# Kernel tuning notes

Hardware: AMD Instinct MI355X
Metric: run time of the kernel (lower is better)

## Reference

```python
import jax, jax.numpy as jnp
import numpy as np

KSIZE = 9
SIGMA = 7.0
ALPHA = 0.05
POOL = 7


def _conv(x, w, pad):
    # x: (N, Cin, H, W), w: (Cout, Cin, kh, kw), zero padding, stride 1
    return jax.lax.conv_general_dilated(
        x, w, window_strides=(1, 1), padding=[(pad, pad), (pad, pad)],
        dimension_numbers=("NCHW", "OIHW", "NCHW"))


def setup_inputs() -> dict:
    key = jax.random.key(0)
    x = jax.random.normal(key, (4, 1, 2048, 2048), dtype=jnp.float32)
    # Sobel filters (ImageGradientsLayer): out ch 0 = Ix, out ch 1 = Iy
    sobel_w = jnp.array(
        [[[[-1., 0., 1.], [-2., 0., 2.], [-1., 0., 1.]]],
         [[[-1., -2., -1.], [0., 0., 0.], [1., 2., 1.]]]], dtype=jnp.float32)
    # Normalized 2D Gaussian kernel, ksize=9, sigma=7
    ax = np.arange(KSIZE) - (KSIZE - 1) / 2.0
    g1 = np.exp(-(ax ** 2) / (2.0 * SIGMA ** 2))
    g2 = np.outer(g1, g1)
    g2 = g2 / g2.sum()
    gauss_w = jnp.asarray(g2, dtype=jnp.float32)[None, None]  # (1,1,9,9)
    return {"x": x, "sobel_w": sobel_w, "gauss_w": gauss_w}


def reference(x, sobel_w, gauss_w):
    # 1) ImageGradientsLayer: Sobel conv -> (N, 2, H, W)
    g = _conv(x, sobel_w, 1)
    Ix, Iy = g[:, 0], g[:, 1]
    # 2) ChannelProductLayer: I_xx, I_yy, I_xy -> (N, 3, H, W)
    prods = jnp.stack([Ix * Ix, Iy * Iy, Ix * Iy], axis=1)
    # 3) SecondMomentMatrixLayer: same 9x9 Gaussian on each channel
    N, C, H, W = prods.shape
    S = _conv(prods.reshape(N * C, 1, H, W), gauss_w, (KSIZE - 1) // 2)
    S = S.reshape(N, C, H, W)
    # 4) CornerResponseLayer: R = det - alpha * trace^2
    det = S[:, 0] * S[:, 1] - S[:, 2] * S[:, 2]
    tr = S[:, 0] + S[:, 1]
    R = (det - ALPHA * tr * tr)[:, None]  # (N, 1, H, W)
    # 5) NMSLayer: global (lower) median threshold, 7x7 maxpool, equality mask
    n = R.size
    med = jnp.sort(R.reshape(-1))[(n - 1) // 2]  # torch.median = lower median
    xt = jnp.where(R > med, R, jnp.zeros_like(R))
    pad = (POOL - 1) // 2
    y = jax.lax.reduce_window(
        xt, -jnp.inf, jax.lax.max, (1, 1, POOL, POOL), (1, 1, 1, 1),
        [(0, 0), (0, 0), (pad, pad), (pad, pad)])
    mask = (xt == y).astype(xt.dtype)
    return mask * xt
```

## Files before the change

### kernel.cpp

```cpp
#include <hip/hip_runtime.h>
#include <cstdint>
#include <math.h>

#define IMH 2048
#define IMW 2048
#define NB 4
#define NPIX (NB*IMH*IMW)
#define MEDRANK ((NPIX-1)/2)
#define ALPHA 0.05f

#define TW 64
#define TH 24
#define XROWS (TH+10)
#define XSTR 84
#define HROWS (TH+8)
#define HSTR 68

__device__ __forceinline__ uint32_t fkey(float f){
  uint32_t u = __float_as_uint(f);
  return (u & 0x80000000u) ? ~u : (u | 0x80000000u);
}
__device__ __forceinline__ uint32_t aload(const uint32_t* p){
  return __hip_atomic_load(p, __ATOMIC_RELAXED, __HIP_MEMORY_SCOPE_AGENT);
}
__device__ __forceinline__ float ldz(const float* __restrict__ p, int r, int c){
  return (r >= 0 && r < IMH && c >= 0 && c < IMW) ? p[(size_t)r*IMW + c] : 0.f;
}

__global__ __launch_bounds__(256) void harris_front(
    const float* __restrict__ x, const float* __restrict__ gauss_w,
    float* __restrict__ R)
{
  __shared__ float xs[XROWS][XSTR];
  __shared__ float hs[3][HROWS][HSTR];

  const int tid = threadIdx.x;
  const int C0 = blockIdx.x * TW;
  const int R0 = blockIdx.y * TH;
  const int n  = blockIdx.z;
  const float* xb = x + (size_t)n * (size_t)(IMH*IMW);

  float ga[9];
  {
    float a4 = sqrtf(gauss_w[4*9+4]);
#pragma unroll
    for (int i = 0; i < 9; i++) ga[i] = gauss_w[4*9+i] / a4;
  }

  for (int u = tid; u < XROWS*20; u += 256){
    int r = u / 20, c4 = u % 20;
    int gr = R0 - 5 + r;
    int gc = C0 - 8 + c4*4;
    float4 v;
    if (gr >= 0 && gr < IMH && gc >= 0 && gc + 3 < IMW){
      v = *reinterpret_cast<const float4*>(&xb[(size_t)gr*IMW + gc]);
    } else {
      v.x = ldz(xb, gr, gc+0); v.y = ldz(xb, gr, gc+1);
      v.z = ldz(xb, gr, gc+2); v.w = ldz(xb, gr, gc+3);
    }
    *reinterpret_cast<float4*>(&xs[r][c4*4]) = v;
  }
  __syncthreads();

  {
    const int hr = tid >> 3;
    const int oc = (tid & 7) * 8;
    const int gr = R0 - 4 + hr;
    const bool rowv = ((unsigned)gr < (unsigned)IMH);

    float ix[16], iy[16];
    {
      float sv[24], dv[24];
#pragma unroll
      for (int m = 0; m < 6; m++){
        float4 a = *reinterpret_cast<const float4*>(&xs[hr  ][oc + m*4]);
        float4 b = *reinterpret_cast<const float4*>(&xs[hr+1][oc + m*4]);
        float4 c = *reinterpret_cast<const float4*>(&xs[hr+2][oc + m*4]);
        sv[m*4+0] = fmaf(2.f, b.x, a.x + c.x);  dv[m*4+0] = c.x - a.x;
        sv[m*4+1] = fmaf(2.f, b.y, a.y + c.y);  dv[m*4+1] = c.y - a.y;
        sv[m*4+2] = fmaf(2.f, b.z, a.z + c.z);  dv[m*4+2] = c.z - a.z;
        sv[m*4+3] = fmaf(2.f, b.w, a.w + c.w);  dv[m*4+3] = c.w - a.w;
      }
#pragma unroll
      for (int j = 0; j < 16; j++){
        float vx = sv[j+5] - sv[j+3];
        float vy = dv[j+3] + fmaf(2.f, dv[j+4], dv[j+5]);
        int gc = C0 + oc - 4 + j;
        bool vld = rowv && ((unsigned)gc < (unsigned)IMW);
        ix[j] = vld ? vx : 0.f;
        iy[j] = vld ? vy : 0.f;
      }
    }
#pragma unroll
    for (int p = 0; p < 3; p++){
      float pr[16];
#pragma unroll
      for (int j = 0; j < 16; j++)
        pr[j] = (p == 0) ? ix[j]*ix[j] : (p == 1) ? iy[j]*iy[j] : ix[j]*iy[j];
      float o[8];
#pragma unroll
      for (int t2 = 0; t2 < 8; t2++){
        float s = 0.f;
#pragma unroll
        for (int k = 0; k < 9; k++) s = fmaf(ga[k], pr[t2+k], s);
        o[t2] = s;
      }
      *reinterpret_cast<float4*>(&hs[p][hr][oc])   = make_float4(o[0],o[1],o[2],o[3]);
      *reinterpret_cast<float4*>(&hs[p][hr][oc+4]) = make_float4(o[4],o[5],o[6],o[7]);
    }
  }
  __syncthreads();

  if (tid < 192){
    const int c4o = tid & 15;
    const int r0o = (tid >> 4) * 2;
    float4 sA[3], sB[3];
#pragma unroll
    for (int p = 0; p < 3; p++){
      float4 a0 = make_float4(0,0,0,0), a1 = make_float4(0,0,0,0);
#pragma unroll
      for (int k = 0; k < 10; k++){
        float4 hv = *reinterpret_cast<const float4*>(&hs[p][r0o+k][c4o*4]);
        if (k < 9){
          a0.x = fmaf(ga[k], hv.x, a0.x); a0.y = fmaf(ga[k], hv.y, a0.y);
          a0.z = fmaf(ga[k], hv.z, a0.z); a0.w = fmaf(ga[k], hv.w, a0.w);
        }
        if (k >= 1){
          a1.x = fmaf(ga[k-1], hv.x, a1.x); a1.y = fmaf(ga[k-1], hv.y, a1.y);
          a1.z = fmaf(ga[k-1], hv.z, a1.z); a1.w = fmaf(ga[k-1], hv.w, a1.w);
        }
      }
      sA[p] = a0; sB[p] = a1;
    }
    float* Rb = R + (size_t)n * (size_t)(IMH*IMW);
    float4 o0, o1;
    float s0, s1, s2, det, tr;
    s0=sA[0].x; s1=sA[1].x; s2=sA[2].x; det=s0*s1-s2*s2; tr=s0+s1; o0.x=det-ALPHA*tr*tr;
    s0=sA[0].y; s1=sA[1].y; s2=sA[2].y; det=s0*s1-s2*s2; tr=s0+s1; o0.y=det-ALPHA*tr*tr;
    s0=sA[0].z; s1=sA[1].z; s2=sA[2].z; det=s0*s1-s2*s2; tr=s0+s1; o0.z=det-ALPHA*tr*tr;
    s0=sA[0].w; s1=sA[1].w; s2=sA[2].w; det=s0*s1-s2*s2; tr=s0+s1; o0.w=det-ALPHA*tr*tr;
    s0=sB[0].x; s1=sB[1].x; s2=sB[2].x; det=s0*s1-s2*s2; tr=s0+s1; o1.x=det-ALPHA*tr*tr;
    s0=sB[0].y; s1=sB[1].y; s2=sB[2].y; det=s0*s1-s2*s2; tr=s0+s1; o1.y=det-ALPHA*tr*tr;
    s0=sB[0].z; s1=sB[1].z; s2=sB[2].z; det=s0*s1-s2*s2; tr=s0+s1; o1.z=det-ALPHA*tr*tr;
    s0=sB[0].w; s1=sB[1].w; s2=sB[2].w; det=s0*s1-s2*s2; tr=s0+s1; o1.w=det-ALPHA*tr*tr;

    const int orow = R0 + r0o;
    const int ocol = C0 + c4o*4;
    if (orow < IMH)
      *reinterpret_cast<float4*>(&Rb[(size_t)orow*IMW + ocol]) = o0;
    if (orow + 1 < IMH)
      *reinterpret_cast<float4*>(&Rb[(size_t)(orow+1)*IMW + ocol]) = o1;
  }
}

#define HREP 32
__global__ __launch_bounds__(256) void harris_hist8(
    const float4* __restrict__ R4, uint32_t* __restrict__ h8,
    uint32_t* __restrict__ state, uint32_t* __restrict__ ctr)
{
  __shared__ uint32_t lh[256*HREP];
  __shared__ uint32_t sc[256];
  __shared__ int lastFlag;
  for (int i = threadIdx.x; i < 256*HREP; i += 256) lh[i] = 0;
  __syncthreads();
  const int copy = threadIdx.x & (HREP-1);
  const int stride = gridDim.x * 256;
  for (int i = blockIdx.x*256 + threadIdx.x; i < NPIX/4; i += stride){
    float4 v = R4[i];
    atomicAdd(&lh[(fkey(v.x) >> 24)*HREP + copy], 1u);
    atomicAdd(&lh[(fkey(v.y) >> 24)*HREP + copy], 1u);
    atomicAdd(&lh[(fkey(v.z) >> 24)*HREP + copy], 1u);
    atomicAdd(&lh[(fkey(v.w) >> 24)*HREP + copy], 1u);
  }
  __syncthreads();
  {
    const int t = threadIdx.x;
    uint32_t s = 0;
#pragma unroll
    for (int i = 0; i < HREP; i++) s += lh[t*HREP + ((t + i) & (HREP-1))];
    if (s) atomicAdd(&h8[t], s);
  }
  __syncthreads();
  if (threadIdx.x == 0){
    __threadfence();
    lastFlag = (atomicAdd(ctr, 1u) == (uint32_t)gridDim.x - 1u);
  }
  __syncthreads();
  if (!lastFlag) return;
  __threadfence();
  const int t = threadIdx.x;
  uint32_t cnt = aload(&h8[t]);
  sc[t] = cnt;
  __syncthreads();
  for (int off = 1; off < 256; off <<= 1){
    uint32_t v = (t >= off) ? sc[t-off] : 0u;
    __syncthreads();
    sc[t] += v;
    __syncthreads();
  }
  uint32_t excl = sc[t] - cnt;
  if ((uint32_t)MEDRANK >= excl && (uint32_t)MEDRANK < excl + cnt){
    state[0] = (uint32_t)t;
    state[1] = (uint32_t)MEDRANK - excl;
  }
}

__global__ __launch_bounds__(256) void harris_hist12(
    const float4* __restrict__ R4, uint32_t* __restrict__ h,
    uint32_t* __restrict__ state, uint32_t* __restrict__ ctr, int phase)
{
  __shared__ uint32_t lh[4096];
  __shared__ uint32_t sc[256];
  __shared__ int lastFlag;
  for (int i = threadIdx.x; i < 4096; i += 256) lh[i] = 0;
  __syncthreads();
  const uint32_t target = (phase == 0) ? state[0] : ((state[0] << 12) | state[2]);
  const int shift = (phase == 0) ? 24 : 12;
  const int stride = gridDim.x * 256;
  for (int i = blockIdx.x*256 + threadIdx.x; i < NPIX/4; i += stride){
    float4 v = R4[i];
    uint32_t k;
    k = fkey(v.x); if ((k >> shift) == target) atomicAdd(&lh[(k >> (shift-12)) & 0xfffu], 1u);
    k = fkey(v.y); if ((k >> shift) == target) atomicAdd(&lh[(k >> (shift-12)) & 0xfffu], 1u);
    k = fkey(v.z); if ((k >> shift) == target) atomicAdd(&lh[(k >> (shift-12)) & 0xfffu], 1u);
    k = fkey(v.w); if ((k >> shift) == target) atomicAdd(&lh[(k >> (shift-12)) & 0xfffu], 1u);
  }
  __syncthreads();
  for (int i = threadIdx.x; i < 4096; i += 256)
    if (lh[i]) atomicAdd(&h[i], lh[i]);
  __syncthreads();
  if (threadIdx.x == 0){
    __threadfence();
    lastFlag = (atomicAdd(ctr, 1u) == (uint32_t)gridDim.x - 1u);
  }
  __syncthreads();
  if (!lastFlag) return;
  __threadfence();
  const int t = threadIdx.x;
  uint32_t vals[16];
  uint32_t lsum = 0;
#pragma unroll
  for (int i = 0; i < 16; i++){ vals[i] = aload(&h[t*16 + i]); lsum += vals[i]; }
  sc[t] = lsum;
  __syncthreads();
  for (int off = 1; off < 256; off <<= 1){
    uint32_t v = (t >= off) ? sc[t-off] : 0u;
    __syncthreads();
    sc[t] += v;
    __syncthreads();
  }
  uint32_t excl = sc[t] - lsum;
  uint32_t rank = (phase == 0) ? state[1] : state[3];
  if (rank >= excl && rank < excl + lsum){
    uint32_t cum = excl;
    for (int i = 0; i < 16; i++){
      if (rank < cum + vals[i]){
        uint32_t bin = (uint32_t)(t*16 + i);
        if (phase == 0){ state[2] = bin; state[3] = rank - cum; }
        else {
          uint32_t key = (state[0] << 24) | (state[2] << 12) | bin;
          uint32_t u = (key & 0x80000000u) ? (key & 0x7fffffffu) : ~key;
          state[4] = u;
        }
        break;
      }
      cum += vals[i];
    }
  }
}

#define PT 64
__global__ __launch_bounds__(256) void harris_nms(
    const float* __restrict__ R, const uint32_t* __restrict__ state,
    float* __restrict__ out)
{
  __shared__ float xt[PT+6][76];
  __shared__ float hm[PT+6][68];

  const int tid = threadIdx.x;
  const int C0 = blockIdx.x * PT;
  const int R0 = blockIdx.y * PT;
  const int n  = blockIdx.z;
  const float med = __uint_as_float(state[4]);
  const float* Rb = R + (size_t)n * (size_t)(IMH*IMW);

  for (int u = tid; u < 70*18; u += 256){
    int r  = u / 18, c4 = u % 18;
    int gr = R0 - 3 + r;
    int gc = C0 - 4 + c4*4;
    float4 v;
    if (gr >= 0 && gr < IMH && gc >= 0 && gc + 3 < IMW){
      v = *reinterpret_cast<const float4*>(&Rb[(size_t)gr*IMW + gc]);
      v.x = v.x > med ? v.x : 0.f;
      v.y = v.y > med ? v.y : 0.f;
      v.z = v.z > med ? v.z : 0.f;
      v.w = v.w > med ? v.w : 0.f;
    } else {
      float t0, t1, t2, t3;
      t0 = (gr>=0&&gr<IMH&&gc+0>=0&&gc+0<IMW) ? Rb[(size_t)gr*IMW+gc+0] : -INFINITY;
      t1 = (gr>=0&&gr<IMH&&gc+1>=0&&gc+1<IMW) ? Rb[(size_t)gr*IMW+gc+1] : -INFINITY;
      t2 = (gr>=0&&gr<IMH&&gc+2>=0&&gc+2<IMW) ? Rb[(size_t)gr*IMW+gc+2] : -INFINITY;
      t3 = (gr>=0&&gr<IMH&&gc+3>=0&&gc+3<IMW) ? Rb[(size_t)gr*IMW+gc+3] : -INFINITY;
      v.x = (t0 == -INFINITY) ? t0 : (t0 > med ? t0 : 0.f);
      v.y = (t1 == -INFINITY) ? t1 : (t1 > med ? t1 : 0.f);
      v.z = (t2 == -INFINITY) ? t2 : (t2 > med ? t2 : 0.f);
      v.w = (t3 == -INFINITY) ? t3 : (t3 > med ? t3 : 0.f);
    }
    *reinterpret_cast<float4*>(&xt[r][c4*4]) = v;
  }
  __syncthreads();

  for (int u = tid; u < 70*16; u += 256){
    int r = u / 16, c4 = u % 16;
    float4 t0 = *reinterpret_cast<const float4*>(&xt[r][c4*4]);
    float4 t1 = *reinterpret_cast<const float4*>(&xt[r][c4*4+4]);
    float4 t2 = *reinterpret_cast<const float4*>(&xt[r][c4*4+8]);
    float w[12];
    w[0]=t0.x; w[1]=t0.y; w[2]=t0.z; w[3]=t0.w;
    w[4]=t1.x; w[5]=t1.y; w[6]=t1.z; w[7]=t1.w;
    w[8]=t2.x; w[9]=t2.y; w[10]=t2.z; w[11]=t2.w;
    float o[4];
#pragma unroll
    for (int j = 0; j < 4; j++){
      float m = w[j+1];
#pragma unroll
      for (int k = 2; k <= 7; k++) m = fmaxf(m, w[j+k]);
      o[j] = m;
    }
    *reinterpret_cast<float4*>(&hm[r][c4*4]) = make_float4(o[0],o[1],o[2],o[3]);
  }
  __syncthreads();

  const int c4o = tid & 15;
  const int r0o = (tid >> 4) * 4;
  float4 hv[10];
#pragma unroll
  for (int k = 0; k < 10; k++)
    hv[k] = *reinterpret_cast<const float4*>(&hm[r0o+k][c4o*4]);

  float* ob = out + (size_t)n * (size_t)(IMH*IMW);
#pragma unroll
  for (int i = 0; i < 4; i++){
    float4 y = hv[i];
#pragma unroll
    for (int k = 1; k < 7; k++){
      float4 t = hv[i+k];
      y.x = fmaxf(y.x, t.x); y.y = fmaxf(y.y, t.y);
      y.z = fmaxf(y.z, t.z); y.w = fmaxf(y.w, t.w);
    }
    float4 c = *reinterpret_cast<const float4*>(&xt[r0o+i+3][c4o*4+4]);
    float4 o;
    o.x = (c.x == y.x) ? c.x : 0.f;
    o.y = (c.y == y.y) ? c.y : 0.f;
    o.z = (c.z == y.z) ? c.z : 0.f;
    o.w = (c.w == y.w) ? c.w : 0.f;
    *reinterpret_cast<float4*>(&ob[(size_t)(R0+r0o+i)*IMW + C0 + c4o*4]) = o;
  }
}

extern "C" void kernel_launch(void* const* d_in, const int* in_sizes, int n_in,
                              void* d_out, int out_size, void* d_ws, size_t ws_size,
                              hipStream_t stream)
{
  (void)in_sizes; (void)n_in; (void)out_size; (void)ws_size;
  const float* x  = (const float*)d_in[0];
  const float* gw = (const float*)d_in[2];
  float* out = (float*)d_out;

  float* R = (float*)d_ws;
  uint32_t* aux   = (uint32_t*)((char*)d_ws + (size_t)NPIX * sizeof(float));
  uint32_t* h8    = aux;
  uint32_t* h12a  = aux + 256;
  uint32_t* h12b  = aux + 256 + 4096;
  uint32_t* state = aux + 256 + 4096 + 4096;
  uint32_t* ctr   = state + 8;

  hipMemsetAsync(aux, 0, (256 + 4096 + 4096 + 8 + 3) * sizeof(uint32_t), stream);

  harris_front<<<dim3(IMW/TW, (IMH + TH - 1)/TH, NB), 256, 0, stream>>>(x, gw, R);

  harris_hist8 <<<1024, 256, 0, stream>>>((const float4*)R, h8, state, ctr);
  harris_hist12<<<1024, 256, 0, stream>>>((const float4*)R, h12a, state, ctr+1, 0);
  harris_hist12<<<1024, 256, 0, stream>>>((const float4*)R, h12b, state, ctr+2, 1);

  harris_nms<<<dim3(IMW/PT, IMH/PT, NB), 256, 0, stream>>>(R, state, out);
}
```

Measured before the change: 342.8 us.

## Fuse histogram passes and NMS into one persistent kernel with grid barriers

Merges the three radix-select histogram kernels and the NMS kernel into a single persistent kernel of 512 blocks. Blocks synchronise through spin-wait grid barriers on global counters instead of separate launches, and the median search state is carried in registers and shared memory. The histogram loops also process two float4 loads per iteration. This removes the launch gaps between kernels and the last-block-done scan logic, but relies on all 512 blocks being co-resident for the spin barriers, and the 8-tile-per-block NMS loop may reduce parallelism.

```diff
diff --git a/kernel.cpp b/kernel.cpp
--- a/kernel.cpp
+++ b/kernel.cpp
@@ -15,6 +15,9 @@
 #define XSTR 84
 #define HROWS (TH+8)
 #define HSTR 68
+
+#define TB 512
+#define HREP 32
 
 __device__ __forceinline__ uint32_t fkey(float f){
   uint32_t u = __float_as_uint(f);
@@ -153,208 +156,280 @@
   }
 }
 
-#define HREP 32
-__global__ __launch_bounds__(256) void harris_hist8(
-    const float4* __restrict__ R4, uint32_t* __restrict__ h8,
-    uint32_t* __restrict__ state, uint32_t* __restrict__ ctr)
+__global__ __launch_bounds__(256) void harris_tail(
+    const float* __restrict__ R, uint32_t* __restrict__ h8,
+    uint32_t* __restrict__ h12a, uint32_t* __restrict__ h12b,
+    uint32_t* __restrict__ ctr, float* __restrict__ out)
 {
-  __shared__ uint32_t lh[256*HREP];
-  __shared__ uint32_t sc[256];
-  __shared__ int lastFlag;
-  for (int i = threadIdx.x; i < 256*HREP; i += 256) lh[i] = 0;
-  __syncthreads();
-  const int copy = threadIdx.x & (HREP-1);
-  const int stride = gridDim.x * 256;
-  for (int i = blockIdx.x*256 + threadIdx.x; i < NPIX/4; i += stride){
-    float4 v = R4[i];
-    atomicAdd(&lh[(fkey(v.x) >> 24)*HREP + copy], 1u);
-    atomicAdd(&lh[(fkey(v.y) >> 24)*HREP + copy], 1u);
-    atomicAdd(&lh[(fkey(v.z) >> 24)*HREP + copy], 1u);
-    atomicAdd(&lh[(fkey(v.w) >> 24)*HREP + copy], 1u);
-  }
-  __syncthreads();
-  {
-    const int t = threadIdx.x;
+  __shared__ uint32_t sm[10080];
+  uint32_t* lh = sm;
+  uint32_t* sc = sm + 8192;
+  uint32_t* bc = sm + 8448;
+
+  const int tid = threadIdx.x;
+  const int bid = blockIdx.x;
+  const float4* R4 = (const float4*)R;
+  const uint32_t stride = TB * 256;
+
+  for (int i = tid; i < 8192; i += 256) lh[i] = 0;
+  __syncthreads();
+  {
+    const int copy = tid & (HREP-1);
+    for (uint32_t i = bid*256 + tid; i < NPIX/4; i += 2*stride){
+      float4 a = R4[i];
+      float4 b = R4[i + stride];
+      atomicAdd(&lh[(fkey(a.x) >> 24)*HREP + copy], 1u);
+      atomicAdd(&lh[(fkey(a.y) >> 24)*HREP + copy], 1u);
+      atomicAdd(&lh[(fkey(a.z) >> 24)*HREP + copy], 1u);
+      atomicAdd(&lh[(fkey(a.w) >> 24)*HREP + copy], 1u);
+      atomicAdd(&lh[(fkey(b.x) >> 24)*HREP + copy], 1u);
+      atomicAdd(&lh[(fkey(b.y) >> 24)*HREP + copy], 1u);
+      atomicAdd(&lh[(fkey(b.z) >> 24)*HREP + copy], 1u);
+      atomicAdd(&lh[(fkey(b.w) >> 24)*HREP + copy], 1u);
+    }
+  }
+  __syncthreads();
+  {
     uint32_t s = 0;
 #pragma unroll
-    for (int i = 0; i < HREP; i++) s += lh[t*HREP + ((t + i) & (HREP-1))];
-    if (s) atomicAdd(&h8[t], s);
-  }
-  __syncthreads();
-  if (threadIdx.x == 0){
+    for (int i = 0; i < HREP; i++) s += lh[tid*HREP + ((tid + i) & (HREP-1))];
+    if (s) atomicAdd(&h8[tid], s);
+  }
+
+  __syncthreads();
+  if (tid == 0){
     __threadfence();
-    lastFlag = (atomicAdd(ctr, 1u) == (uint32_t)gridDim.x - 1u);
-  }
-  __syncthreads();
-  if (!lastFlag) return;
-  __threadfence();
-  const int t = threadIdx.x;
-  uint32_t cnt = aload(&h8[t]);
-  sc[t] = cnt;
-  __syncthreads();
-  for (int off = 1; off < 256; off <<= 1){
-    uint32_t v = (t >= off) ? sc[t-off] : 0u;
-    __syncthreads();
-    sc[t] += v;
-    __syncthreads();
-  }
-  uint32_t excl = sc[t] - cnt;
-  if ((uint32_t)MEDRANK >= excl && (uint32_t)MEDRANK < excl + cnt){
-    state[0] = (uint32_t)t;
-    state[1] = (uint32_t)MEDRANK - excl;
-  }
-}
-
-__global__ __launch_bounds__(256) void harris_hist12(
-    const float4* __restrict__ R4, uint32_t* __restrict__ h,
-    uint32_t* __restrict__ state, uint32_t* __restrict__ ctr, int phase)
-{
-  __shared__ uint32_t lh[4096];
-  __shared__ uint32_t sc[256];
-  __shared__ int lastFlag;
-  for (int i = threadIdx.x; i < 4096; i += 256) lh[i] = 0;
-  __syncthreads();
-  const uint32_t target = (phase == 0) ? state[0] : ((state[0] << 12) | state[2]);
-  const int shift = (phase == 0) ? 24 : 12;
-  const int stride = gridDim.x * 256;
-  for (int i = blockIdx.x*256 + threadIdx.x; i < NPIX/4; i += stride){
-    float4 v = R4[i];
+    __hip_atomic_fetch_add(ctr, 1u, __ATOMIC_RELEASE, __HIP_MEMORY_SCOPE_AGENT);
+    while (__hip_atomic_load(ctr, __ATOMIC_ACQUIRE, __HIP_MEMORY_SCOPE_AGENT) < (uint32_t)TB)
+      __builtin_amdgcn_s_sleep(2);
+  }
+  __syncthreads();
+
+  uint32_t b1, r1;
+  {
+    uint32_t c = aload(&h8[tid]);
+    sc[tid] = c;
+    __syncthreads();
+    for (int off = 1; off < 256; off <<= 1){
+      uint32_t v = (tid >= off) ? sc[tid-off] : 0u;
+      __syncthreads();
+      sc[tid] += v;
+      __syncthreads();
+    }
+    uint32_t excl = sc[tid] - c;
+    if ((uint32_t)MEDRANK >= excl && (uint32_t)MEDRANK < excl + c){
+      bc[0] = (uint32_t)tid;
+      bc[1] = (uint32_t)MEDRANK - excl;
+    }
+    __syncthreads();
+    b1 = bc[0]; r1 = bc[1];
+  }
+
+  __syncthreads();
+  for (int i = tid; i < 4096; i += 256) lh[i] = 0;
+  __syncthreads();
+  for (uint32_t i = bid*256 + tid; i < NPIX/4; i += 2*stride){
+    float4 a = R4[i];
+    float4 b = R4[i + stride];
     uint32_t k;
-    k = fkey(v.x); if ((k >> shift) == target) atomicAdd(&lh[(k >> (shift-12)) & 0xfffu], 1u);
-    k = fkey(v.y); if ((k >> shift) == target) atomicAdd(&lh[(k >> (shift-12)) & 0xfffu], 1u);
-    k = fkey(v.z); if ((k >> shift) == target) atomicAdd(&lh[(k >> (shift-12)) & 0xfffu], 1u);
-    k = fkey(v.w); if ((k >> shift) == target) atomicAdd(&lh[(k >> (shift-12)) & 0xfffu], 1u);
-  }
-  __syncthreads();
-  for (int i = threadIdx.x; i < 4096; i += 256)
-    if (lh[i]) atomicAdd(&h[i], lh[i]);
-  __syncthreads();
-  if (threadIdx.x == 0){
+    k = fkey(a.x); if ((k >> 24) == b1) atomicAdd(&lh[(k >> 12) & 0xfffu], 1u);
+    k = fkey(a.y); if ((k >> 24) == b1) atomicAdd(&lh[(k >> 12) & 0xfffu], 1u);
+    k = fkey(a.z); if ((k >> 24) == b1) atomicAdd(&lh[(k >> 12) & 0xfffu], 1u);
+    k = fkey(a.w); if ((k >> 24) == b1) atomicAdd(&lh[(k >> 12) & 0xfffu], 1u);
+    k = fkey(b.x); if ((k >> 24) == b1) atomicAdd(&lh[(k >> 12) & 0xfffu], 1u);
+    k = fkey(b.y); if ((k >> 24) == b1) atomicAdd(&lh[(k >> 12) & 0xfffu], 1u);
+    k = fkey(b.z); if ((k >> 24) == b1) atomicAdd(&lh[(k >> 12) & 0xfffu], 1u);
+    k = fkey(b.w); if ((k >> 24) == b1) atomicAdd(&lh[(k >> 12) & 0xfffu], 1u);
+  }
+  __syncthreads();
+  for (int i = tid; i < 4096; i += 256)
+    if (lh[i]) atomicAdd(&h12a[i], lh[i]);
+
+  __syncthreads();
+  if (tid == 0){
     __threadfence();
-    lastFlag = (atomicAdd(ctr, 1u) == (uint32_t)gridDim.x - 1u);
-  }
-  __syncthreads();
-  if (!lastFlag) return;
-  __threadfence();
-  const int t = threadIdx.x;
-  uint32_t vals[16];
-  uint32_t lsum = 0;
-#pragma unroll
-  for (int i = 0; i < 16; i++){ vals[i] = aload(&h[t*16 + i]); lsum += vals[i]; }
-  sc[t] = lsum;
-  __syncthreads();
-  for (int off = 1; off < 256; off <<= 1){
-    uint32_t v = (t >= off) ? sc[t-off] : 0u;
-    __syncthreads();
-    sc[t] += v;
-    __syncthreads();
-  }
-  uint32_t excl = sc[t] - lsum;
-  uint32_t rank = (phase == 0) ? state[1] : state[3];
-  if (rank >= excl && rank < excl + lsum){
-    uint32_t cum = excl;
-    for (int i = 0; i < 16; i++){
-      if (rank < cum + vals[i]){
-        uint32_t bin = (uint32_t)(t*16 + i);
-        if (phase == 0){ state[2] = bin; state[3] = rank - cum; }
-        else {
-          uint32_t key = (state[0] << 24) | (state[2] << 12) | bin;
-          uint32_t u = (key & 0x80000000u) ? (key & 0x7fffffffu) : ~key;
-          state[4] = u;
+    __hip_atomic_fetch_add(ctr+1, 1u, __ATOMIC_RELEASE, __HIP_MEMORY_SCOPE_AGENT);
+    while (__hip_atomic_load(ctr+1, __ATOMIC_ACQUIRE, __HIP_MEMORY_SCOPE_AGENT) < (uint32_t)TB)
+      __builtin_amdgcn_s_sleep(2);
+  }
+  __syncthreads();
+
+  uint32_t b2, r2;
+  {
+    uint32_t vals[16];
+    uint32_t lsum = 0;
+#pragma unroll
+    for (int i = 0; i < 16; i++){ vals[i] = aload(&h12a[tid*16 + i]); lsum += vals[i]; }
+    sc[tid] = lsum;
+    __syncthreads();
+    for (int off = 1; off < 256; off <<= 1){
+      uint32_t v = (tid >= off) ? sc[tid-off] : 0u;
+      __syncthreads();
+      sc[tid] += v;
+      __syncthreads();
+    }
+    uint32_t excl = sc[tid] - lsum;
+    if (r1 >= excl && r1 < excl + lsum){
+      uint32_t cum = excl;
+      for (int i = 0; i < 16; i++){
+        if (r1 < cum + vals[i]){
+          bc[2] = (uint32_t)(tid*16 + i);
+          bc[3] = r1 - cum;
+          break;
         }
-        break;
-      }
-      cum += vals[i];
-    }
-  }
-}
-
-#define PT 64
-__global__ __launch_bounds__(256) void harris_nms(
-    const float* __restrict__ R, const uint32_t* __restrict__ state,
-    float* __restrict__ out)
-{
-  __shared__ float xt[PT+6][76];
-  __shared__ float hm[PT+6][68];
-
-  const int tid = threadIdx.x;
-  const int C0 = blockIdx.x * PT;
-  const int R0 = blockIdx.y * PT;
-  const int n  = blockIdx.z;
-  const float med = __uint_as_float(state[4]);
-  const float* Rb = R + (size_t)n * (size_t)(IMH*IMW);
-
-  for (int u = tid; u < 70*18; u += 256){
-    int r  = u / 18, c4 = u % 18;
-    int gr = R0 - 3 + r;
-    int gc = C0 - 4 + c4*4;
-    float4 v;
-    if (gr >= 0 && gr < IMH && gc >= 0 && gc + 3 < IMW){
-      v = *reinterpret_cast<const float4*>(&Rb[(size_t)gr*IMW + gc]);
-      v.x = v.x > med ? v.x : 0.f;
-      v.y = v.y > med ? v.y : 0.f;
-      v.z = v.z > med ? v.z : 0.f;
-      v.w = v.w > med ? v.w : 0.f;
-    } else {
-      float t0, t1, t2, t3;
-      t0 = (gr>=0&&gr<IMH&&gc+0>=0&&gc+0<IMW) ? Rb[(size_t)gr*IMW+gc+0] : -INFINITY;
-      t1 = (gr>=0&&gr<IMH&&gc+1>=0&&gc+1<IMW) ? Rb[(size_t)gr*IMW+gc+1] : -INFINITY;
-      t2 = (gr>=0&&gr<IMH&&gc+2>=0&&gc+2<IMW) ? Rb[(size_t)gr*IMW+gc+2] : -INFINITY;
-      t3 = (gr>=0&&gr<IMH&&gc+3>=0&&gc+3<IMW) ? Rb[(size_t)gr*IMW+gc+3] : -INFINITY;
-      v.x = (t0 == -INFINITY) ? t0 : (t0 > med ? t0 : 0.f);
-      v.y = (t1 == -INFINITY) ? t1 : (t1 > med ? t1 : 0.f);
-      v.z = (t2 == -INFINITY) ? t2 : (t2 > med ? t2 : 0.f);
-      v.w = (t3 == -INFINITY) ? t3 : (t3 > med ? t3 : 0.f);
-    }
-    *reinterpret_cast<float4*>(&xt[r][c4*4]) = v;
-  }
-  __syncthreads();
-
-  for (int u = tid; u < 70*16; u += 256){
-    int r = u / 16, c4 = u % 16;
-    float4 t0 = *reinterpret_cast<const float4*>(&xt[r][c4*4]);
-    float4 t1 = *reinterpret_cast<const float4*>(&xt[r][c4*4+4]);
-    float4 t2 = *reinterpret_cast<const float4*>(&xt[r][c4*4+8]);
-    float w[12];
-    w[0]=t0.x; w[1]=t0.y; w[2]=t0.z; w[3]=t0.w;
-    w[4]=t1.x; w[5]=t1.y; w[6]=t1.z; w[7]=t1.w;
-    w[8]=t2.x; w[9]=t2.y; w[10]=t2.z; w[11]=t2.w;
-    float o[4];
-#pragma unroll
-    for (int j = 0; j < 4; j++){
-      float m = w[j+1];
-#pragma unroll
-      for (int k = 2; k <= 7; k++) m = fmaxf(m, w[j+k]);
-      o[j] = m;
-    }
-    *reinterpret_cast<float4*>(&hm[r][c4*4]) = make_float4(o[0],o[1],o[2],o[3]);
-  }
-  __syncthreads();
-
-  const int c4o = tid & 15;
-  const int r0o = (tid >> 4) * 4;
-  float4 hv[10];
-#pragma unroll
-  for (int k = 0; k < 10; k++)
-    hv[k] = *reinterpret_cast<const float4*>(&hm[r0o+k][c4o*4]);
-
-  float* ob = out + (size_t)n * (size_t)(IMH*IMW);
-#pragma unroll
-  for (int i = 0; i < 4; i++){
-    float4 y = hv[i];
-#pragma unroll
-    for (int k = 1; k < 7; k++){
-      float4 t = hv[i+k];
-      y.x = fmaxf(y.x, t.x); y.y = fmaxf(y.y, t.y);
-      y.z = fmaxf(y.z, t.z); y.w = fmaxf(y.w, t.w);
-    }
-    float4 c = *reinterpret_cast<const float4*>(&xt[r0o+i+3][c4o*4+4]);
-    float4 o;
-    o.x = (c.x == y.x) ? c.x : 0.f;
-    o.y = (c.y == y.y) ? c.y : 0.f;
-    o.z = (c.z == y.z) ? c.z : 0.f;
-    o.w = (c.w == y.w) ? c.w : 0.f;
-    *reinterpret_cast<float4*>(&ob[(size_t)(R0+r0o+i)*IMW + C0 + c4o*4]) = o;
+        cum += vals[i];
+      }
+    }
+    __syncthreads();
+    b2 = bc[2]; r2 = bc[3];
+  }
+
+  __syncthreads();
+  for (int i = tid; i < 4096; i += 256) lh[i] = 0;
+  __syncthreads();
+  {
+    const uint32_t target = (b1 << 12) | b2;
+    for (uint32_t i = bid*256 + tid; i < NPIX/4; i += 2*stride){
+      float4 a = R4[i];
+      float4 b = R4[i + stride];
+      uint32_t k;
+      k = fkey(a.x); if ((k >> 12) == target) atomicAdd(&lh[k & 0xfffu], 1u);
+      k = fkey(a.y); if ((k >> 12) == target) atomicAdd(&lh[k & 0xfffu], 1u);
+      k = fkey(a.z); if ((k >> 12) == target) atomicAdd(&lh[k & 0xfffu], 1u);
+      k = fkey(a.w); if ((k >> 12) == target) atomicAdd(&lh[k & 0xfffu], 1u);
+      k = fkey(b.x); if ((k >> 12) == target) atomicAdd(&lh[k & 0xfffu], 1u);
+      k = fkey(b.y); if ((k >> 12) == target) atomicAdd(&lh[k & 0xfffu], 1u);
+      k = fkey(b.z); if ((k >> 12) == target) atomicAdd(&lh[k & 0xfffu], 1u);
+      k = fkey(b.w); if ((k >> 12) == target) atomicAdd(&lh[k & 0xfffu], 1u);
+    }
+  }
+  __syncthreads();
+  for (int i = tid; i < 4096; i += 256)
+    if (lh[i]) atomicAdd(&h12b[i], lh[i]);
+
+  __syncthreads();
+  if (tid == 0){
+    __threadfence();
+    __hip_atomic_fetch_add(ctr+2, 1u, __ATOMIC_RELEASE, __HIP_MEMORY_SCOPE_AGENT);
+    while (__hip_atomic_load(ctr+2, __ATOMIC_ACQUIRE, __HIP_MEMORY_SCOPE_AGENT) < (uint32_t)TB)
+      __builtin_amdgcn_s_sleep(2);
+  }
+  __syncthreads();
+
+  float med;
+  {
+    uint32_t vals[16];
+    uint32_t lsum = 0;
+#pragma unroll
+    for (int i = 0; i < 16; i++){ vals[i] = aload(&h12b[tid*16 + i]); lsum += vals[i]; }
+    sc[tid] = lsum;
+    __syncthreads();
+    for (int off = 1; off < 256; off <<= 1){
+      uint32_t v = (tid >= off) ? sc[tid-off] : 0u;
+      __syncthreads();
+      sc[tid] += v;
+      __syncthreads();
+    }
+    uint32_t excl = sc[tid] - lsum;
+    if (r2 >= excl && r2 < excl + lsum){
+      uint32_t cum = excl;
+      for (int i = 0; i < 16; i++){
+        if (r2 < cum + vals[i]){
+          uint32_t key = (b1 << 24) | (b2 << 12) | (uint32_t)(tid*16 + i);
+          bc[0] = (key & 0x80000000u) ? (key & 0x7fffffffu) : ~key;
+          break;
+        }
+        cum += vals[i];
+      }
+    }
+    __syncthreads();
+    med = __uint_as_float(bc[0]);
+  }
+
+  float* xt = (float*)sm;
+  float* hm = (float*)(sm + 5320);
+
+  for (int it = 0; it < 8; ++it){
+    const int tile = bid + TB*it;
+    const int C0 = (tile & 31) * 64;
+    const int R0 = ((tile >> 5) & 31) * 64;
+    const int n  = tile >> 10;
+    const float* Rb = R + (size_t)n * (size_t)(IMH*IMW);
+
+    __syncthreads();
+
+    for (int u = tid; u < 70*18; u += 256){
+      int r  = u / 18, c4 = u % 18;
+      int gr = R0 - 3 + r;
+      int gc = C0 - 4 + c4*4;
+      float4 v;
+      if (gr >= 0 && gr < IMH && gc >= 0 && gc + 3 < IMW){
+        v = *reinterpret_cast<const float4*>(&Rb[(size_t)gr*IMW + gc]);
+        v.x = v.x > med ? v.x : 0.f;
+        v.y = v.y > med ? v.y : 0.f;
+        v.z = v.z > med ? v.z : 0.f;
+        v.w = v.w > med ? v.w : 0.f;
+      } else {
+        float t0, t1, t2, t3;
+        t0 = (gr>=0&&gr<IMH&&gc+0>=0&&gc+0<IMW) ? Rb[(size_t)gr*IMW+gc+0] : -INFINITY;
+        t1 = (gr>=0&&gr<IMH&&gc+1>=0&&gc+1<IMW) ? Rb[(size_t)gr*IMW+gc+1] : -INFINITY;
+        t2 = (gr>=0&&gr<IMH&&gc+2>=0&&gc+2<IMW) ? Rb[(size_t)gr*IMW+gc+2] : -INFINITY;
+        t3 = (gr>=0&&gr<IMH&&gc+3>=0&&gc+3<IMW) ? Rb[(size_t)gr*IMW+gc+3] : -INFINITY;
+        v.x = (t0 == -INFINITY) ? t0 : (t0 > med ? t0 : 0.f);
+        v.y = (t1 == -INFINITY) ? t1 : (t1 > med ? t1 : 0.f);
+        v.z = (t2 == -INFINITY) ? t2 : (t2 > med ? t2 : 0.f);
+        v.w = (t3 == -INFINITY) ? t3 : (t3 > med ? t3 : 0.f);
+      }
+      *reinterpret_cast<float4*>(&xt[r*76 + c4*4]) = v;
+    }
+    __syncthreads();
+
+    for (int u = tid; u < 70*16; u += 256){
+      int r = u / 16, c4 = u % 16;
+      float4 t0 = *reinterpret_cast<const float4*>(&xt[r*76 + c4*4]);
+      float4 t1 = *reinterpret_cast<const float4*>(&xt[r*76 + c4*4+4]);
+      float4 t2 = *reinterpret_cast<const float4*>(&xt[r*76 + c4*4+8]);
+      float w[12];
+      w[0]=t0.x; w[1]=t0.y; w[2]=t0.z; w[3]=t0.w;
+      w[4]=t1.x; w[5]=t1.y; w[6]=t1.z; w[7]=t1.w;
+      w[8]=t2.x; w[9]=t2.y; w[10]=t2.z; w[11]=t2.w;
+      float o[4];
+#pragma unroll
+      for (int j = 0; j < 4; j++){
+        float m = w[j+1];
+#pragma unroll
+        for (int k = 2; k <= 7; k++) m = fmaxf(m, w[j+k]);
+        o[j] = m;
+      }
+      *reinterpret_cast<float4*>(&hm[r*68 + c4*4]) = make_float4(o[0],o[1],o[2],o[3]);
+    }
+    __syncthreads();
+
+    const int c4o = tid & 15;
+    const int r0o = (tid >> 4) * 4;
+    float4 hv[10];
+#pragma unroll
+    for (int k = 0; k < 10; k++)
+      hv[k] = *reinterpret_cast<const float4*>(&hm[(r0o+k)*68 + c4o*4]);
+
+    float* ob = out + (size_t)n * (size_t)(IMH*IMW);
+#pragma unroll
+    for (int i = 0; i < 4; i++){
+      float4 y = hv[i];
+#pragma unroll
+      for (int k = 1; k < 7; k++){
+        float4 t = hv[i+k];
+        y.x = fmaxf(y.x, t.x); y.y = fmaxf(y.y, t.y);
+        y.z = fmaxf(y.z, t.z); y.w = fmaxf(y.w, t.w);
+      }
+      float4 c = *reinterpret_cast<const float4*>(&xt[(r0o+i+3)*76 + c4o*4+4]);
+      float4 o;
+      o.x = (c.x == y.x) ? c.x : 0.f;
+      o.y = (c.y == y.y) ? c.y : 0.f;
+      o.z = (c.z == y.z) ? c.z : 0.f;
+      o.w = (c.w == y.w) ? c.w : 0.f;
+      *reinterpret_cast<float4*>(&ob[(size_t)(R0+r0o+i)*IMW + C0 + c4o*4]) = o;
+    }
   }
 }
 
@@ -372,16 +447,11 @@
   uint32_t* h8    = aux;
   uint32_t* h12a  = aux + 256;
   uint32_t* h12b  = aux + 256 + 4096;
-  uint32_t* state = aux + 256 + 4096 + 4096;
-  uint32_t* ctr   = state + 8;
-
-  hipMemsetAsync(aux, 0, (256 + 4096 + 4096 + 8 + 3) * sizeof(uint32_t), stream);
+  uint32_t* ctr   = aux + 256 + 4096 + 4096;
+
+  hipMemsetAsync(aux, 0, (256 + 4096 + 4096 + 4) * sizeof(uint32_t), stream);
 
   harris_front<<<dim3(IMW/TW, (IMH + TH - 1)/TH, NB), 256, 0, stream>>>(x, gw, R);
 
-  harris_hist8 <<<1024, 256, 0, stream>>>((const float4*)R, h8, state, ctr);
-  harris_hist12<<<1024, 256, 0, stream>>>((const float4*)R, h12a, state, ctr+1, 0);
-  harris_hist12<<<1024, 256, 0, stream>>>((const float4*)R, h12b, state, ctr+2, 1);
-
-  harris_nms<<<dim3(IMW/PT, IMH/PT, NB), 256, 0, stream>>>(R, state, out);
-}
+  harris_tail<<<TB, 256, 0, stream>>>(R, h8, h12a, h12b, ctr, out);
+}
```

After: 437.6 us. 27.7% more time.
